# Kernel tuning notes

Hardware: AMD Instinct MI355X
Metric: run time of the kernel (lower is better)

Reference implementation:

```python
import jax, jax.numpy as jnp
import numpy as np

B, S, D = 2, 2048, 2048
H = 16
Q_LORA, KV_LORA = 1536, 512
ROPE_DIM, NOPE_DIM, V_DIM = 64, 64, 128
Q_HEAD_DIM = NOPE_DIM + ROPE_DIM  # 128
ROPE_THETA, ROPE_RATIO = 10000.0, 1.0


def setup_inputs() -> dict:
    key = jax.random.key(0)
    ks = jax.random.split(key, 6)
    std = 0.02
    return {
        "hidden_states": jax.random.normal(ks[0], (B, S, D), jnp.float32),
        "Wqa": jax.random.normal(ks[1], (D, Q_LORA), jnp.float32) * std,
        "Wqb": jax.random.normal(ks[2], (Q_LORA, H * Q_HEAD_DIM), jnp.float32) * std,
        "Wkva": jax.random.normal(ks[3], (D, KV_LORA + ROPE_DIM), jnp.float32) * std,
        "Wkvb": jax.random.normal(ks[4], (KV_LORA, H * (NOPE_DIM + V_DIM)), jnp.float32) * std,
        "Wo": jax.random.normal(ks[5], (H * V_DIM, D), jnp.float32) * std,
    }


def _rope_tables(seq_len):
    half = ROPE_DIM // 2
    inv_freq = ROPE_RATIO / (ROPE_THETA ** (jnp.arange(half, dtype=jnp.float32) * 2.0 / ROPE_DIM))
    freqs = jnp.arange(seq_len, dtype=jnp.float32)[:, None] * inv_freq[None, :]  # [S, half]
    return jnp.cos(freqs), jnp.sin(freqs)


def _apply_rope(x, cos, sin):
    # interleaved even/odd rotation, matches torch stack+flatten
    x_even = x[..., 0::2]
    x_odd = x[..., 1::2]
    r_even = x_even * cos - x_odd * sin
    r_odd = x_odd * cos + x_even * sin
    return jnp.stack([r_even, r_odd], axis=-1).reshape(x.shape)


def reference(hidden_states, Wqa, Wqb, Wkva, Wkvb, Wo):
    b, s, _ = hidden_states.shape
    scale = Q_HEAD_DIM ** -0.5

    # query compression path
    q_latent = hidden_states @ Wqa                             # [B,S,Q_LORA]
    q = (q_latent @ Wqb).reshape(b, s, H, Q_HEAD_DIM)
    q = jnp.transpose(q, (0, 2, 1, 3))                          # [B,H,S,q_head_dim]
    q_nope, q_pe = q[..., :NOPE_DIM], q[..., NOPE_DIM:]

    # kv compression
    kv_comp = hidden_states @ Wkva                              # [B,S,KV_LORA+ROPE]
    c_kv, k_pe = kv_comp[..., :KV_LORA], kv_comp[..., KV_LORA:]

    cos, sin = _rope_tables(s)                                  # [S, ROPE_DIM//2]
    q_pe = _apply_rope(q_pe, cos, sin)                          # [B,H,S,ROPE]
    k_pe = _apply_rope(k_pe, cos, sin)                          # [B,S,ROPE]

    # kv decompression
    kv = (c_kv @ Wkvb).reshape(b, s, H, NOPE_DIM + V_DIM)
    kv = jnp.transpose(kv, (0, 2, 1, 3))                        # [B,H,S,nope+v]
    k_nope, v = kv[..., :NOPE_DIM], kv[..., NOPE_DIM:]

    k_pe_b = jnp.broadcast_to(k_pe[:, None], (b, H, s, ROPE_DIM))
    q_full = jnp.concatenate([q_nope, q_pe], axis=-1)           # [B,H,S,128]
    k_full = jnp.concatenate([k_nope, k_pe_b], axis=-1)         # [B,H,S,128]

    scores = jnp.einsum('bhqd,bhkd->bhqk', q_full, k_full) * scale
    causal = jnp.tril(jnp.ones((s, s), dtype=bool))
    scores = jnp.where(causal[None, None], scores, jnp.finfo(scores.dtype).min)
    probs = jax.nn.softmax(scores, axis=-1)
    attn = jnp.einsum('bhqk,bhkd->bhqd', probs, v)              # [B,H,S,V_DIM]

    out = jnp.transpose(attn, (0, 2, 1, 3)).reshape(b, s, H * V_DIM)
    return out @ Wo                                             # [B,S,D]
```

## Files before the change

kernel.cpp:

```cpp
#include <hip/hip_runtime.h>
#include <hip/hip_bf16.h>
#include <cstdint>
#include <cstddef>

typedef __bf16 bf16_t;
typedef __attribute__((ext_vector_type(4))) __bf16 bf16x4;
typedef __attribute__((ext_vector_type(8))) __bf16 bf16x8;
typedef __attribute__((ext_vector_type(4))) float f32x4;

#define S_ 2048
#define H_ 16
#define NTOK 4096

__device__ __forceinline__ f32x4 mfma16x16(bf16x8 a, bf16x8 b, f32x4 c) {
  return __builtin_amdgcn_mfma_f32_16x16x32_bf16(a, b, c, 0, 0, 0);
}
__device__ __forceinline__ bf16x8 load8(const bf16_t* p) {
  return *reinterpret_cast<const bf16x8*>(p);
}
__device__ __forceinline__ void load_lds16(const void* g, void* l) {
  __builtin_amdgcn_global_load_lds(
      (const __attribute__((address_space(1))) uint32_t*)g,
      (__attribute__((address_space(3))) uint32_t*)l, 16, 0, 0);
}


__global__ void cast_bf16_k(const float* __restrict__ in, bf16_t* __restrict__ out, int n) {
  int idx = blockIdx.x * 256 + threadIdx.x;
  int i4 = idx * 4;
  if (i4 >= n) return;
  float4 v = *reinterpret_cast<const float4*>(in + i4);
  out[i4 + 0] = (bf16_t)v.x;
  out[i4 + 1] = (bf16_t)v.y;
  out[i4 + 2] = (bf16_t)v.z;
  out[i4 + 3] = (bf16_t)v.w;
}

__global__ void rope_tables_k(float* __restrict__ cosT, float* __restrict__ sinT) {
  int idx = blockIdx.x * 256 + threadIdx.x;
  if (idx >= S_ * 32) return;
  int s = idx >> 5, i = idx & 31;
  float inv = powf(10000.0f, -(2.0f * (float)i) / 64.0f);
  float fr = (float)s * inv;
  cosT[idx] = cosf(fr);
  sinT[idx] = sinf(fr);
}

struct TDesc {
  const float* src;
  bf16_t* dst;
  int K, Nsrc, bxc, off, perm;
};
struct TDesc5 {
  TDesc d[5];
};

__global__ void transpose_cast_multi_k(TDesc5 ds) {
  __shared__ float tile[32][33];
  const int bid = blockIdx.x;
  int i = 0;
#pragma unroll
  for (int j = 1; j < 5; ++j)
    if (bid >= ds.d[j].off) i = j;
  const float* __restrict__ in = ds.d[i].src;
  bf16_t* __restrict__ out = ds.d[i].dst;
  const int K = ds.d[i].K, Nsrc = ds.d[i].Nsrc;
  const int local = bid - ds.d[i].off;
  const int n0 = (local % ds.d[i].bxc) * 32;
  const int k0 = (local / ds.d[i].bxc) * 32;
  int srcn0 = n0;
  if (ds.d[i].perm) {
    srcn0 = (n0 < 1024) ? ((n0 >> 6) * 192 + (n0 & 63))
                        : (((n0 - 1024) >> 7) * 192 + 64 + ((n0 - 1024) & 127));
  }
  int tx = threadIdx.x & 31, ty = threadIdx.x >> 5;
#pragma unroll
  for (int r = 0; r < 4; ++r) {
    int k = k0 + ty + r * 8, n = srcn0 + tx;
    tile[ty + r * 8][tx] = (n < Nsrc) ? in[(size_t)k * Nsrc + n] : 0.0f;
  }
  __syncthreads();
#pragma unroll
  for (int r = 0; r < 4; ++r) {
    int n = n0 + ty + r * 8, k = k0 + tx;
    out[(size_t)n * K + k] = (bf16_t)tile[tx][ty + r * 8];
  }
}


__device__ __forceinline__ void gemm_loop64(const bf16_t* __restrict__ A, int lda,
                                            const bf16_t* __restrict__ Bt, int K, int m0, int n0,
                                            int tid, bf16_t* Al, bf16_t* Bl, f32x4 (&acc)[4][4]) {
  const int wid = tid >> 6, lane = tid & 63;
  const int wm = (wid >> 1) * 64, wn = (wid & 1) * 64;
  const int srow8 = lane >> 3, c8 = lane & 7;
  const int swz8 = c8 ^ srow8;
  const int lr = lane & 15, lg = lane >> 4;
  const int e = lr & 7;

  const bf16_t* ag = A + (size_t)(m0 + wid * 32 + srow8) * lda + (swz8 << 3);
  const bf16_t* bg = Bt + (size_t)(n0 + wid * 32 + srow8) * K + (swz8 << 3);

  for (int k0 = 0; k0 < K; k0 += 64) {
#pragma unroll
    for (int rr = 0; rr < 4; ++rr) {
      load_lds16(ag + (size_t)(rr * 8) * lda + k0, &Al[(wid * 32 + rr * 8) * 64]);
      load_lds16(bg + (size_t)(rr * 8) * K + k0, &Bl[(wid * 32 + rr * 8) * 64]);
    }
    __syncthreads();
#pragma unroll
    for (int kk = 0; kk < 2; ++kk) {
      bf16x8 af[4], bfr[4];
#pragma unroll
      for (int i = 0; i < 4; ++i) {
        af[i] = load8(&Al[(wm + i * 16 + lr) * 64 + (((kk * 4 + lg) ^ e) << 3)]);
        bfr[i] = load8(&Bl[(wn + i * 16 + lr) * 64 + (((kk * 4 + lg) ^ e) << 3)]);
      }
#pragma unroll
      for (int i = 0; i < 4; ++i)
#pragma unroll
        for (int j = 0; j < 4; ++j) acc[i][j] = mfma16x16(af[i], bfr[j], acc[i][j]);
    }
    __syncthreads();
  }
}


__global__ __launch_bounds__(256) void gemm_lat_k(const bf16_t* __restrict__ A,
                                                  const bf16_t* __restrict__ Bt,
                                                  bf16_t* __restrict__ C,
                                                  const float* __restrict__ cosT,
                                                  const float* __restrict__ sinT) {
  __shared__ alignas(16) bf16_t Al[128 * 64];
  __shared__ alignas(16) bf16_t Bl[128 * 64];
  const int tid = threadIdx.x;
  const int sw = (blockIdx.x & 7) * 68 + (blockIdx.x >> 3);
  const int m0 = (sw / 17) * 128, n0 = (sw % 17) * 128;
  f32x4 acc[4][4] = {};
  gemm_loop64(A, 2048, Bt, 2048, m0, n0, tid, Al, Bl, acc);

  const int wid = tid >> 6, lane = tid & 63;
  const int wm = (wid >> 1) * 64, wn = (wid & 1) * 64;
  const int lr = lane & 15, lg = lane >> 4;
  const bool rope = (n0 == 2048) && (wn == 0);
  const int ir_base = lr >> 1;
  const bool odd = lane & 1;
#pragma unroll
  for (int i = 0; i < 4; ++i)
#pragma unroll
    for (int j = 0; j < 4; ++j) {
      float v4[4];
#pragma unroll
      for (int r = 0; r < 4; ++r) v4[r] = acc[i][j][r];
      if (rope) {
        const int ir = j * 8 + ir_base;
#pragma unroll
        for (int r = 0; r < 4; ++r) {
          const int srow_ = (m0 + wm + i * 16 + lg * 4 + r) & (S_ - 1);
          float c = cosT[srow_ * 32 + ir], sn = sinT[srow_ * 32 + ir];
          float partner = __shfl_xor(v4[r], 1);
          v4[r] = odd ? (v4[r] * c + partner * sn) : (v4[r] * c - partner * sn);
        }
      }
#pragma unroll
      for (int r = 0; r < 4; ++r) {
        int row = m0 + wm + i * 16 + lg * 4 + r;
        int col = n0 + wn + j * 16 + lr;
        C[(size_t)row * 2176 + col] = (bf16_t)v4[r];
      }
    }
}


__global__ __launch_bounds__(256) void gemm_qkv_k(const bf16_t* __restrict__ lat,
                                                  const bf16_t* __restrict__ Wqbt,
                                                  const bf16_t* __restrict__ Wkvbt,
                                                  bf16_t* __restrict__ qb,
                                                  bf16_t* __restrict__ knb,
                                                  bf16_t* __restrict__ vT,
                                                  const float* __restrict__ cosT,
                                                  const float* __restrict__ sinT, float qscale) {
  __shared__ alignas(16) bf16_t Al[128 * 64];
  __shared__ alignas(16) bf16_t Bl[128 * 64];
  const int tid = threadIdx.x;
  const int sw = (blockIdx.x & 7) * 160 + (blockIdx.x >> 3);
  const int wid = tid >> 6, lane = tid & 63;
  const int wm = (wid >> 1) * 64, wn = (wid & 1) * 64;
  const int lr = lane & 15, lg = lane >> 4;
  f32x4 acc[4][4] = {};

  if (sw < 512) {
    const int m0 = (sw >> 4) * 128, n0 = (sw & 15) * 128;
    gemm_loop64(lat, 2176, Wqbt, 1536, m0, n0, tid, Al, Bl, acc);
    const bool rope = (wn == 64);
    const int ir_base = lr >> 1;
    const bool odd = lane & 1;
#pragma unroll
    for (int i = 0; i < 4; ++i)
#pragma unroll
      for (int j = 0; j < 4; ++j) {
        float v4[4];
#pragma unroll
        for (int r = 0; r < 4; ++r) v4[r] = acc[i][j][r] * qscale;
        if (rope) {
          const int ir = j * 8 + ir_base;
#pragma unroll
          for (int r = 0; r < 4; ++r) {
            const int srow_ = (m0 + wm + i * 16 + lg * 4 + r) & (S_ - 1);
            float c = cosT[srow_ * 32 + ir], sn = sinT[srow_ * 32 + ir];
            float partner = __shfl_xor(v4[r], 1);
            v4[r] = odd ? (v4[r] * c + partner * sn) : (v4[r] * c - partner * sn);
          }
        }
#pragma unroll
        for (int r = 0; r < 4; ++r) {
          int row = m0 + wm + i * 16 + lg * 4 + r;
          int col = n0 + wn + j * 16 + lr;
          qb[(size_t)row * 2048 + col] = (bf16_t)v4[r];
        }
      }
  } else {
    const int b2 = sw - 512;
    const int m0 = (b2 / 24) * 128, n0 = (b2 % 24) * 128;
    gemm_loop64(lat + 1536, 2176, Wkvbt, 512, m0, n0, tid, Al, Bl, acc);
    if (n0 < 1024) {
#pragma unroll
      for (int i = 0; i < 4; ++i)
#pragma unroll
        for (int j = 0; j < 4; ++j)
#pragma unroll
          for (int r = 0; r < 4; ++r) {
            int row = m0 + wm + i * 16 + lg * 4 + r;
            int col = n0 + wn + j * 16 + lr;
            knb[(size_t)row * 1024 + col] = (bf16_t)acc[i][j][r];
          }
    } else {
#pragma unroll
      for (int i = 0; i < 4; ++i) {
        const int row0 = m0 + wm + i * 16 + lg * 4;
        const int bb = row0 >> 11;
        const int s0 = row0 & (S_ - 1);
#pragma unroll
        for (int j = 0; j < 4; ++j) {
          const int idx = n0 + wn + j * 16 + lr - 1024;
          const int h = idx >> 7, d = idx & 127;
          bf16x4 pk;
#pragma unroll
          for (int r = 0; r < 4; ++r) pk[r] = (bf16_t)acc[i][j][r];
          *reinterpret_cast<bf16x4*>(&vT[((size_t)(bb * 16 + h) * 128 + d) * 2048 + s0]) = pk;
        }
      }
    }
  }
}


__global__ __launch_bounds__(256) void gemm_out_k(const bf16_t* __restrict__ A,
                                                  const bf16_t* __restrict__ Bt,
                                                  float* __restrict__ C) {
  __shared__ alignas(16) bf16_t Al[128 * 64];
  __shared__ alignas(16) bf16_t Bl[128 * 64];
  const int tid = threadIdx.x;
  const int sw = (blockIdx.x & 7) * 64 + (blockIdx.x >> 3);
  const int m0 = (sw >> 4) * 128, n0 = (sw & 15) * 128;
  f32x4 acc[4][4] = {};
  gemm_loop64(A, 2048, Bt, 2048, m0, n0, tid, Al, Bl, acc);
  const int wid = tid >> 6, lane = tid & 63;
  const int wm = (wid >> 1) * 64, wn = (wid & 1) * 64;
  const int lr = lane & 15, lg = lane >> 4;
#pragma unroll
  for (int i = 0; i < 4; ++i)
#pragma unroll
    for (int j = 0; j < 4; ++j)
#pragma unroll
      for (int r = 0; r < 4; ++r) {
        int row = m0 + wm + i * 16 + lg * 4 + r;
        int col = n0 + wn + j * 16 + lr;
        C[(size_t)row * 2048 + col] = acc[i][j][r];
      }
}

__global__ __launch_bounds__(256) void attn_fused(const bf16_t* __restrict__ q,
                                                  const bf16_t* __restrict__ knb,
                                                  const bf16_t* __restrict__ lat,
                                                  const bf16_t* __restrict__ vT,
                                                  bf16_t* __restrict__ out) {
  __shared__ alignas(16) bf16_t Kn[64 * 64];
  __shared__ alignas(16) bf16_t Kp[64 * 64];
  __shared__ alignas(16) bf16_t Vt[128 * 64];
  __shared__ alignas(16) bf16_t Pl[4][16 * 64];
  const int tid = threadIdx.x, wid = tid >> 6, lane = tid & 63;
  const int bid = blockIdx.x;
  const int g = bid >> 8;
  const int x = (bid >> 5) & 7;
  const int bh = bid & 31;
  const int qt = (g & 1) ? (24 - g * 8 + x) : (31 - g * 8 - x);
  const int b = bh >> 4, h = bh & 15;
  const int tokb = b * S_;
  const int lr = lane & 15, lg = lane >> 4;
  const int srow8 = lane >> 3, c8 = lane & 7;
  const int swz8 = c8 ^ srow8;
  bf16_t* Pw = &Pl[wid][0];

  bf16x8 ones;
#pragma unroll
  for (int j = 0; j < 8; ++j) ones[j] = (bf16_t)1.0f;

  bf16x8 qf[4];
  {
    const int qrow = qt * 64 + wid * 16 + lr;
    const bf16_t* qp = q + (size_t)(tokb + qrow) * 2048 + h * 128 + lg * 8;
#pragma unroll
    for (int ds = 0; ds < 4; ++ds) qf[ds] = load8(qp + ds * 32);
  }

  f32x4 o[8] = {};
  f32x4 o8 = {};
  float mrow[4] = {-1e30f, -1e30f, -1e30f, -1e30f};

  for (int t = 0; t <= qt; ++t) {
    const int kb = t * 64;
#pragma unroll
    for (int rr = 0; rr < 2; ++rr) {
      const int r0 = wid * 16 + rr * 8;
      const size_t tk = (size_t)(tokb + kb + r0 + srow8);
      load_lds16(knb + tk * 1024 + h * 64 + (swz8 << 3), &Kn[r0 * 64]);
      load_lds16(lat + tk * 2176 + 2048 + (swz8 << 3), &Kp[r0 * 64]);
    }
#pragma unroll
    for (int rr = 0; rr < 4; ++rr) {
      const int r0 = wid * 32 + rr * 8;
      load_lds16(vT + ((size_t)bh * 128 + r0 + srow8) * 2048 + kb + (swz8 << 3), &Vt[r0 * 64]);
    }
    __syncthreads();

    f32x4 s[4];
    __builtin_amdgcn_s_setprio(1);
#pragma unroll
    for (int kt = 0; kt < 4; ++kt) {
      const int row = kt * 16 + lr;
      const int e = lr & 7;
      bf16x8 kf0 = load8(&Kn[row * 64 + ((lg ^ e) << 3)]);
      bf16x8 kf1 = load8(&Kn[row * 64 + (((lg + 4) ^ e) << 3)]);
      bf16x8 kf2 = load8(&Kp[row * 64 + ((lg ^ e) << 3)]);
      bf16x8 kf3 = load8(&Kp[row * 64 + (((lg + 4) ^ e) << 3)]);
      f32x4 acc = {0.f, 0.f, 0.f, 0.f};
      acc = mfma16x16(qf[0], kf0, acc);
      acc = mfma16x16(qf[1], kf1, acc);
      acc = mfma16x16(qf[2], kf2, acc);
      acc = mfma16x16(qf[3], kf3, acc);
      s[kt] = acc;
    }
    __builtin_amdgcn_s_setprio(0);

    if (t == qt) {
#pragma unroll
      for (int kt = 0; kt < 4; ++kt) {
        const int key = kb + kt * 16 + lr;
#pragma unroll
        for (int r = 0; r < 4; ++r) {
          const int qr = qt * 64 + wid * 16 + lg * 4 + r;
          if (key > qr) s[kt][r] = -1e30f;
        }
      }
    }

    float tm[4];
#pragma unroll
    for (int r = 0; r < 4; ++r) {
      float mx = fmaxf(fmaxf(s[0][r], s[1][r]), fmaxf(s[2][r], s[3][r]));
      mx = fmaxf(mx, __shfl_xor(mx, 1));
      mx = fmaxf(mx, __shfl_xor(mx, 2));
      mx = fmaxf(mx, __shfl_xor(mx, 4));
      mx = fmaxf(mx, __shfl_xor(mx, 8));
      tm[r] = mx;
    }
    float need = fmaxf(fmaxf(tm[0] - mrow[0], tm[1] - mrow[1]),
                       fmaxf(tm[2] - mrow[2], tm[3] - mrow[3]));
    if (!__all(need <= 8.0f)) {
#pragma unroll
      for (int r = 0; r < 4; ++r) {
        float mn = fmaxf(mrow[r], tm[r]);
        float corr = exp2f(mrow[r] - mn);
        mrow[r] = mn;
        o8[r] *= corr;
#pragma unroll
        for (int n = 0; n < 8; ++n) o[n][r] *= corr;
      }
    }
#pragma unroll
    for (int kt = 0; kt < 4; ++kt)
#pragma unroll
      for (int r = 0; r < 4; ++r) s[kt][r] = exp2f(s[kt][r] - mrow[r]);

#pragma unroll
    for (int kt = 0; kt < 4; ++kt)
#pragma unroll
      for (int r = 0; r < 4; ++r) {
        const int qrow = lg * 4 + r;
        const int key = kt * 16 + lr;
        Pw[qrow * 64 + ((((key >> 3) ^ (qrow & 7)) << 3) | (key & 7))] = (bf16_t)s[kt][r];
      }

    __builtin_amdgcn_s_setprio(1);
#pragma unroll
    for (int ks = 0; ks < 2; ++ks) {
      const int e = lr & 7;
      bf16x8 pa = load8(&Pw[lr * 64 + (((ks * 4 + lg) ^ e) << 3)]);
#pragma unroll
      for (int n = 0; n < 8; ++n) {
        bf16x8 vb = load8(&Vt[(n * 16 + lr) * 64 + (((ks * 4 + lg) ^ e) << 3)]);
        o[n] = mfma16x16(pa, vb, o[n]);
      }
      o8 = mfma16x16(pa, ones, o8);
    }
    __builtin_amdgcn_s_setprio(0);
    __syncthreads();
  }

  float linv[4];
#pragma unroll
  for (int r = 0; r < 4; ++r) linv[r] = __builtin_amdgcn_rcpf(o8[r]);
#pragma unroll
  for (int n = 0; n < 8; ++n)
#pragma unroll
    for (int r = 0; r < 4; ++r) {
      const int qr = qt * 64 + wid * 16 + lg * 4 + r;
      out[(size_t)(tokb + qr) * 2048 + h * 128 + n * 16 + lr] = (bf16_t)(o[n][r] * linv[r]);
    }
}


extern "C" void kernel_launch(void* const* d_in, const int* in_sizes, int n_in, void* d_out,
                              int out_size, void* d_ws, size_t ws_size, hipStream_t stream) {
  const float* hs = (const float*)d_in[0];
  const float* Wqa = (const float*)d_in[1];
  const float* Wqb = (const float*)d_in[2];
  const float* Wkva = (const float*)d_in[3];
  const float* Wkvb = (const float*)d_in[4];
  const float* Wo = (const float*)d_in[5];
  float* out = (float*)d_out;

  char* ws = (char*)d_ws;
  size_t off = 0;
  auto alloc = [&](size_t bytes) {
    void* p = ws + off;
    off += (bytes + 255) & ~(size_t)255;
    return p;
  };
  bf16_t* hsb = (bf16_t*)alloc((size_t)NTOK * 2048 * 2);
  bf16_t* W1t = (bf16_t*)alloc((size_t)2176 * 2048 * 2);
  bf16_t* Wqbt = (bf16_t*)alloc((size_t)2048 * 1536 * 2);
  bf16_t* Wkvbt = (bf16_t*)alloc((size_t)3072 * 512 * 2);
  bf16_t* Wot = (bf16_t*)alloc((size_t)2048 * 2048 * 2);
  bf16_t* lat = (bf16_t*)alloc((size_t)NTOK * 2176 * 2);
  bf16_t* qb = (bf16_t*)alloc((size_t)NTOK * 2048 * 2);
  bf16_t* knb = (bf16_t*)alloc((size_t)NTOK * 1024 * 2);
  bf16_t* attn = (bf16_t*)alloc((size_t)NTOK * 2048 * 2);
  bf16_t* vT = (bf16_t*)alloc((size_t)32 * 128 * 2048 * 2);
  float* cosT = (float*)alloc((size_t)S_ * 32 * 4);
  float* sinT = (float*)alloc((size_t)S_ * 32 * 4);

  cast_bf16_k<<<(NTOK * 2048 / 4 + 255) / 256, 256, 0, stream>>>(hs, hsb, NTOK * 2048);
  rope_tables_k<<<(S_ * 32 + 255) / 256, 256, 0, stream>>>(cosT, sinT);
  {
    TDesc5 ds;
    int o0 = 0;
    auto add = [&](int i, const float* src, bf16_t* dst, int K, int Nsrc, int Nout, int perm) {
      int bxc = Nout / 32, cnt = bxc * (K / 32);
      ds.d[i] = TDesc{src, dst, K, Nsrc, bxc, o0, perm};
      o0 += cnt;
    };
    add(0, Wqa, W1t, 2048, 1536, 1536, 0);
    add(1, Wkva, W1t + (size_t)1536 * 2048, 2048, 576, 640, 0);
    add(2, Wqb, Wqbt, 1536, 2048, 2048, 0);
    add(3, Wkvb, Wkvbt, 512, 3072, 3072, 1);
    add(4, Wo, Wot, 2048, 2048, 2048, 0);
    transpose_cast_multi_k<<<o0, 256, 0, stream>>>(ds);
  }

  gemm_lat_k<<<dim3(544), 256, 0, stream>>>(hsb, W1t, lat, cosT, sinT);
  const float scale = 0.08838834764831845f * 1.4426950408889634f;
  gemm_qkv_k<<<dim3(1280), 256, 0, stream>>>(lat, Wqbt, Wkvbt, qb, knb, vT, cosT, sinT, scale);
  attn_fused<<<dim3(1024), 256, 0, stream>>>(qb, knb, lat, vT, attn);
  gemm_out_k<<<dim3(512), 256, 0, stream>>>(attn, Wot, out);
}
```

Measured before the change: 305.4 us.

## Double-buffer LDS tiles in GEMM loop and interleave q/kv block scheduling

The shared GEMM main loop now uses two LDS buffers per operand and prefetches the next K-slice with global_load_lds while the current slice feeds the MFMAs, using explicit vmcnt waits and raw s_barriers instead of __syncthreads. This is meant to hide global-load latency behind compute. The qkv kernel also remaps block indices so Q-projection tiles (K=1536) and KV tiles (K=512) are interleaved 2:3, which should balance the long and short blocks across the machine. LDS use per block doubles to 64 KB, which may reduce how many blocks fit on each CU.

```diff
diff --git a/kernel.cpp b/kernel.cpp
--- a/kernel.cpp
+++ b/kernel.cpp
@@ -101,27 +101,47 @@
   const bf16_t* ag = A + (size_t)(m0 + wid * 32 + srow8) * lda + (swz8 << 3);
   const bf16_t* bg = Bt + (size_t)(n0 + wid * 32 + srow8) * K + (swz8 << 3);
 
+  auto STAGE = [&](int buf, int k0) {
+    bf16_t* ab = Al + buf * (128 * 64);
+    bf16_t* bb = Bl + buf * (128 * 64);
+#pragma unroll
+    for (int rr = 0; rr < 4; ++rr) {
+      load_lds16(ag + (size_t)(rr * 8) * lda + k0, &ab[(wid * 32 + rr * 8) * 64]);
+      load_lds16(bg + (size_t)(rr * 8) * K + k0, &bb[(wid * 32 + rr * 8) * 64]);
+    }
+  };
+
+  STAGE(0, 0);
+  int cur = 0;
   for (int k0 = 0; k0 < K; k0 += 64) {
-#pragma unroll
-    for (int rr = 0; rr < 4; ++rr) {
-      load_lds16(ag + (size_t)(rr * 8) * lda + k0, &Al[(wid * 32 + rr * 8) * 64]);
-      load_lds16(bg + (size_t)(rr * 8) * K + k0, &Bl[(wid * 32 + rr * 8) * 64]);
-    }
-    __syncthreads();
+    if (k0 + 64 < K) {
+      STAGE(cur ^ 1, k0 + 64);
+      __builtin_amdgcn_sched_barrier(0);
+      asm volatile("s_waitcnt vmcnt(8)" ::: "memory");
+    } else {
+      asm volatile("s_waitcnt vmcnt(0)" ::: "memory");
+    }
+    __builtin_amdgcn_sched_barrier(0);
+    __builtin_amdgcn_s_barrier();
+    __builtin_amdgcn_sched_barrier(0);
+    const bf16_t* Ab = Al + cur * (128 * 64);
+    const bf16_t* Bb = Bl + cur * (128 * 64);
 #pragma unroll
     for (int kk = 0; kk < 2; ++kk) {
       bf16x8 af[4], bfr[4];
 #pragma unroll
       for (int i = 0; i < 4; ++i) {
-        af[i] = load8(&Al[(wm + i * 16 + lr) * 64 + (((kk * 4 + lg) ^ e) << 3)]);
-        bfr[i] = load8(&Bl[(wn + i * 16 + lr) * 64 + (((kk * 4 + lg) ^ e) << 3)]);
+        af[i] = load8(&Ab[(wm + i * 16 + lr) * 64 + (((kk * 4 + lg) ^ e) << 3)]);
+        bfr[i] = load8(&Bb[(wn + i * 16 + lr) * 64 + (((kk * 4 + lg) ^ e) << 3)]);
       }
 #pragma unroll
       for (int i = 0; i < 4; ++i)
 #pragma unroll
         for (int j = 0; j < 4; ++j) acc[i][j] = mfma16x16(af[i], bfr[j], acc[i][j]);
     }
-    __syncthreads();
+    __builtin_amdgcn_sched_barrier(0);
+    __builtin_amdgcn_s_barrier();
+    cur ^= 1;
   }
 }
 
@@ -131,8 +151,8 @@
                                                   bf16_t* __restrict__ C,
                                                   const float* __restrict__ cosT,
                                                   const float* __restrict__ sinT) {
-  __shared__ alignas(16) bf16_t Al[128 * 64];
-  __shared__ alignas(16) bf16_t Bl[128 * 64];
+  __shared__ alignas(16) bf16_t Al[2 * 128 * 64];
+  __shared__ alignas(16) bf16_t Bl[2 * 128 * 64];
   const int tid = threadIdx.x;
   const int sw = (blockIdx.x & 7) * 68 + (blockIdx.x >> 3);
   const int m0 = (sw / 17) * 128, n0 = (sw % 17) * 128;
@@ -180,17 +200,19 @@
                                                   bf16_t* __restrict__ vT,
                                                   const float* __restrict__ cosT,
                                                   const float* __restrict__ sinT, float qscale) {
-  __shared__ alignas(16) bf16_t Al[128 * 64];
-  __shared__ alignas(16) bf16_t Bl[128 * 64];
+  __shared__ alignas(16) bf16_t Al[2 * 128 * 64];
+  __shared__ alignas(16) bf16_t Bl[2 * 128 * 64];
   const int tid = threadIdx.x;
   const int sw = (blockIdx.x & 7) * 160 + (blockIdx.x >> 3);
   const int wid = tid >> 6, lane = tid & 63;
   const int wm = (wid >> 1) * 64, wn = (wid & 1) * 64;
   const int lr = lane & 15, lg = lane >> 4;
   f32x4 acc[4][4] = {};
-
-  if (sw < 512) {
-    const int m0 = (sw >> 4) * 128, n0 = (sw & 15) * 128;
+  const int r5 = sw % 5, q5 = sw / 5;
+
+  if (r5 < 2) {
+    const int qi = q5 * 2 + r5;
+    const int m0 = (qi >> 4) * 128, n0 = (qi & 15) * 128;
     gemm_loop64(lat, 2176, Wqbt, 1536, m0, n0, tid, Al, Bl, acc);
     const bool rope = (wn == 64);
     const int ir_base = lr >> 1;
@@ -220,8 +242,8 @@
         }
       }
   } else {
-    const int b2 = sw - 512;
-    const int m0 = (b2 / 24) * 128, n0 = (b2 % 24) * 128;
+    const int ki = q5 * 3 + (r5 - 2);
+    const int m0 = (ki / 24) * 128, n0 = (ki % 24) * 128;
     gemm_loop64(lat + 1536, 2176, Wkvbt, 512, m0, n0, tid, Al, Bl, acc);
     if (n0 < 1024) {
 #pragma unroll
@@ -258,8 +280,8 @@
 __global__ __launch_bounds__(256) void gemm_out_k(const bf16_t* __restrict__ A,
                                                   const bf16_t* __restrict__ Bt,
                                                   float* __restrict__ C) {
-  __shared__ alignas(16) bf16_t Al[128 * 64];
-  __shared__ alignas(16) bf16_t Bl[128 * 64];
+  __shared__ alignas(16) bf16_t Al[2 * 128 * 64];
+  __shared__ alignas(16) bf16_t Bl[2 * 128 * 64];
   const int tid = threadIdx.x;
   const int sw = (blockIdx.x & 7) * 64 + (blockIdx.x >> 3);
   const int m0 = (sw >> 4) * 128, n0 = (sw & 15) * 128;
```

Result: faster. 286.0 us (-6.3%).
